# Kernel tuning notes

Hardware: AMD Instinct MI355X
Metric: run time of the kernel (lower is better)

The kernel has to match this reference:

```python
import jax, jax.numpy as jnp
import numpy as np


def setup_inputs() -> dict:
    key = jax.random.key(0)
    ks = jax.random.split(key, 8)
    B, N, A, H = 2, 2048, 256, 8
    KD = A // H  # key_dim per head = 32
    VD = A // H  # value_dim per head = 32
    return {
        "q_data": jax.random.normal(ks[0], (B, N, A), dtype=jnp.float32),
        "bias": jax.random.normal(ks[1], (B, N), dtype=jnp.float32),
        "nonbatched_bias": jax.random.normal(ks[2], (H, N, N), dtype=jnp.float32),
        "query_w": jax.random.normal(ks[3], (A, H, KD), dtype=jnp.float32) * 0.05,
        "query_b": jax.random.normal(ks[4], (1, H, KD), dtype=jnp.float32) * 0.05,
        "key_w": jax.random.normal(ks[5], (A, H, KD), dtype=jnp.float32) * 0.05,
        "value_w": jax.random.normal(ks[6], (A, H, VD), dtype=jnp.float32) * 0.05,
        "gating_w": jax.random.normal(ks[7], (A, H, VD), dtype=jnp.float32) * 0.05,
    }


def reference(q_data, bias, nonbatched_bias, query_w, query_b, key_w, value_w, gating_w):
    # q_data: [b, n, a]; bias: [b, n_k]; nonbatched_bias: [h, n_q, n_k]
    key_dim = query_w.shape[-1]
    scale = key_dim ** (-0.5)
    # projections (fused QKV in the original kernel)
    q = (jnp.einsum("bqa,ahc->bqhc", q_data, query_w) + query_b) * scale  # [b,q,h,c]
    k = jnp.einsum("bka,ahc->bkhc", q_data, key_w)                        # [b,k,h,c]
    v = jnp.einsum("bka,ahv->bkhv", q_data, value_w)                      # [b,k,h,v]
    # attention logits + batched bias (over keys) + shared nonbatched bias
    logits = jnp.einsum("bqhc,bkhc->bhqk", q, k)
    logits = logits + bias[:, None, None, :] + nonbatched_bias[None]
    weights = jax.nn.softmax(logits, axis=-1)                             # [b,h,q,k]
    weighted = jnp.einsum("bhqk,bkhv->bqhv", weights, v)                  # [b,q,h,v]
    # sigmoid gating branch fused after value projection
    gate = jax.nn.sigmoid(jnp.einsum("bqa,ahv->bqhv", q_data, gating_w))
    return weighted * gate                                                # [b,q,h,v]
```

## Files before the change

### kernel.cpp

```cpp
#include <hip/hip_runtime.h>
#include <stdint.h>

#define NTOK 2048
#define SCALE 0.17677669529663687f

typedef short s16x8 __attribute__((ext_vector_type(8)));
typedef unsigned short u16x8 __attribute__((ext_vector_type(8)));
typedef float f32x4 __attribute__((ext_vector_type(4)));

__device__ __forceinline__ unsigned short f2bf(float f) {
  unsigned int u = __builtin_bit_cast(unsigned int, f);
  u += 0x7fffu + ((u >> 16) & 1u);
  return (unsigned short)(u >> 16);
}

__global__ __launch_bounds__(256) void prep_weights_k(
    const float* __restrict__ qw, const float* __restrict__ kw,
    const float* __restrict__ vw, const float* __restrict__ gw,
    unsigned short* __restrict__ Wt) {
  __shared__ float tile[64][68];
  const int p = blockIdx.z;
  const int a0 = blockIdx.x * 64;
  const int n0 = blockIdx.y * 64;
  const float* src = (p == 0) ? qw : (p == 1) ? kw : (p == 2) ? vw : gw;
  const int tx = threadIdx.x & 15;
  const int ty = threadIdx.x >> 4;
#pragma unroll
  for (int kk = 0; kk < 4; kk++) {
    int ar = ty + kk * 16;
    float4 v = *reinterpret_cast<const float4*>(src + (a0 + ar) * 256 + n0 + tx * 4);
    tile[ar][tx * 4 + 0] = v.x; tile[ar][tx * 4 + 1] = v.y;
    tile[ar][tx * 4 + 2] = v.z; tile[ar][tx * 4 + 3] = v.w;
  }
  __syncthreads();
  unsigned short* dst = Wt + p * 65536;
#pragma unroll
  for (int kk = 0; kk < 4; kk++) {
    int nr = ty + kk * 16;
    ushort4 o;
    o.x = f2bf(tile[tx * 4 + 0][nr]);
    o.y = f2bf(tile[tx * 4 + 1][nr]);
    o.z = f2bf(tile[tx * 4 + 2][nr]);
    o.w = f2bf(tile[tx * 4 + 3][nr]);
    *reinterpret_cast<ushort4*>(dst + (n0 + nr) * 256 + a0 + tx * 4) = o;
  }
}

__global__ __launch_bounds__(256) void proj_k(
    const float* __restrict__ x, const unsigned short* __restrict__ Wt,
    const float* __restrict__ query_b,
    unsigned short* __restrict__ Qg, unsigned short* __restrict__ Kg,
    unsigned short* __restrict__ Vt, float* __restrict__ gate) {
  const int w = threadIdx.x >> 6;
  const int lane = threadIdx.x & 63;
  const int l15 = lane & 15;
  const int quad = lane >> 4;
  const int p = blockIdx.y >> 1;
  const int half = blockIdx.y & 1;
  const int rbase = blockIdx.x * 128 + w * 32;
  const unsigned short* wp = Wt + p * 65536;

  f32x4 acc[2][8];
#pragma unroll
  for (int rt = 0; rt < 2; rt++)
#pragma unroll
    for (int ct = 0; ct < 8; ct++) acc[rt][ct] = (f32x4){0.f, 0.f, 0.f, 0.f};

  for (int ks = 0; ks < 8; ks++) {
    const int kb = ks * 32;
    s16x8 af[2];
#pragma unroll
    for (int rt = 0; rt < 2; rt++) {
      const float* xr = x + (rbase + rt * 16 + l15) * 256 + kb + quad * 8;
      float4 f0 = *reinterpret_cast<const float4*>(xr);
      float4 f1 = *reinterpret_cast<const float4*>(xr + 4);
      u16x8 t;
      t[0] = f2bf(f0.x); t[1] = f2bf(f0.y); t[2] = f2bf(f0.z); t[3] = f2bf(f0.w);
      t[4] = f2bf(f1.x); t[5] = f2bf(f1.y); t[6] = f2bf(f1.z); t[7] = f2bf(f1.w);
      af[rt] = __builtin_bit_cast(s16x8, t);
    }
#pragma unroll
    for (int ct = 0; ct < 8; ct++) {
      uint4 bv = *reinterpret_cast<const uint4*>(
          wp + (half * 128 + ct * 16 + l15) * 256 + kb + quad * 8);
      s16x8 bfr = __builtin_bit_cast(s16x8, bv);
#pragma unroll
      for (int rt = 0; rt < 2; rt++)
        acc[rt][ct] = __builtin_amdgcn_mfma_f32_16x16x32_bf16(af[rt], bfr, acc[rt][ct], 0, 0, 0);
    }
  }

#pragma unroll
  for (int ct = 0; ct < 8; ct++) {
    const int cgl = half * 128 + ct * 16 + l15;
    const int h = cgl >> 5, c = cgl & 31;
#pragma unroll
    for (int rt = 0; rt < 2; rt++) {
      const int n0r = rbase + rt * 16 + quad * 4;
      const int bidx = n0r >> 11;
      const int nl0 = n0r & 2047;
      if (p == 0) {
        const float qb = query_b[cgl];
#pragma unroll
        for (int i = 0; i < 4; i++) {
          float v = (acc[rt][ct][i] + qb) * SCALE;
          Qg[(size_t)((bidx * 8 + h) * 2048 + nl0 + i) * 32 + c] = f2bf(v);
        }
      } else if (p == 1) {
#pragma unroll
        for (int i = 0; i < 4; i++)
          Kg[(size_t)((bidx * 8 + h) * 2048 + nl0 + i) * 32 + c] = f2bf(acc[rt][ct][i]);
      } else if (p == 2) {
        ushort4 o;
        o.x = f2bf(acc[rt][ct][0]); o.y = f2bf(acc[rt][ct][1]);
        o.z = f2bf(acc[rt][ct][2]); o.w = f2bf(acc[rt][ct][3]);
        *reinterpret_cast<ushort4*>(Vt + (size_t)((bidx * 8 + h) * 32 + c) * 2048 + nl0) = o;
      } else {
#pragma unroll
        for (int i = 0; i < 4; i++) {
          float s = 1.f / (1.f + __expf(-acc[rt][ct][i]));
          gate[(size_t)(bidx * 2048 + nl0 + i) * 256 + cgl] = s;
        }
      }
    }
  }
}

#define PST 136
__global__ __launch_bounds__(128) void attn_k(
    const unsigned short* __restrict__ Qg, const unsigned short* __restrict__ Kg,
    const unsigned short* __restrict__ Vt, const float* __restrict__ bias,
    const float* __restrict__ nb, const float* __restrict__ gate,
    float* __restrict__ out) {
  __shared__ unsigned short Ps[2 * 32 * PST];
  const int w = threadIdx.x >> 6;
  const int lane = threadIdx.x & 63;
  const int l15 = lane & 15;
  const int quad = lane >> 4;
  const int h = blockIdx.y, b = blockIdx.z;
  const int bh = b * 8 + h;
  const int qbase = blockIdx.x * 64 + w * 32;
  const unsigned short* Qp = Qg + (size_t)bh * 2048 * 32;
  const unsigned short* Kp = Kg + (size_t)bh * 2048 * 32;
  const unsigned short* Vp = Vt + (size_t)bh * 32 * 2048;
  const float* nbp = nb + (size_t)h * 2048 * 2048;
  const float* biasp = bias + b * 2048;
  unsigned short* Pw = Ps + w * 32 * PST;

  s16x8 aq[2];
#pragma unroll
  for (int rt = 0; rt < 2; rt++)
    aq[rt] = __builtin_bit_cast(s16x8, *reinterpret_cast<const uint4*>(
        Qp + (size_t)(qbase + rt * 16 + l15) * 32 + quad * 8));

  float mst[2][4], lst[2][4];
  f32x4 o[2][2];
#pragma unroll
  for (int rt = 0; rt < 2; rt++)
#pragma unroll
    for (int i = 0; i < 4; i++) { mst[rt][i] = -INFINITY; lst[rt][i] = 0.f; }
#pragma unroll
  for (int rt = 0; rt < 2; rt++)
#pragma unroll
    for (int vt = 0; vt < 2; vt++) o[rt][vt] = (f32x4){0.f, 0.f, 0.f, 0.f};

  for (int kt = 0; kt < 16; kt++) {
    const int kb = kt * 128;
    s16x8 bk[8];
#pragma unroll
    for (int ct = 0; ct < 8; ct++)
      bk[ct] = __builtin_bit_cast(s16x8, *reinterpret_cast<const uint4*>(
          Kp + (size_t)(kb + ct * 16 + l15) * 32 + quad * 8));
    f32x4 s[2][8];
#pragma unroll
    for (int rt = 0; rt < 2; rt++)
#pragma unroll
      for (int ct = 0; ct < 8; ct++)
        s[rt][ct] = __builtin_amdgcn_mfma_f32_16x16x32_bf16(
            aq[rt], bk[ct], (f32x4){0.f, 0.f, 0.f, 0.f}, 0, 0, 0);

    float bcol[8];
#pragma unroll
    for (int ct = 0; ct < 8; ct++) bcol[ct] = biasp[kb + ct * 16 + l15];

#pragma unroll
    for (int rt = 0; rt < 2; rt++) {
      const int qr0 = qbase + rt * 16 + quad * 4;
      float nbv[8][4];
#pragma unroll
      for (int ct = 0; ct < 8; ct++)
#pragma unroll
        for (int i = 0; i < 4; i++)
          nbv[ct][i] = nbp[(size_t)(qr0 + i) * 2048 + kb + ct * 16 + l15];
#pragma unroll
      for (int ct = 0; ct < 8; ct++)
#pragma unroll
        for (int i = 0; i < 4; i++) s[rt][ct][i] += bcol[ct] + nbv[ct][i];

      float alpha[4];
#pragma unroll
      for (int i = 0; i < 4; i++) {
        float mx = s[rt][0][i];
#pragma unroll
        for (int ct = 1; ct < 8; ct++) mx = fmaxf(mx, s[rt][ct][i]);
        mx = fmaxf(mx, __shfl_xor(mx, 1));
        mx = fmaxf(mx, __shfl_xor(mx, 2));
        mx = fmaxf(mx, __shfl_xor(mx, 4));
        mx = fmaxf(mx, __shfl_xor(mx, 8));
        float mn = fmaxf(mst[rt][i], mx);
        alpha[i] = __expf(mst[rt][i] - mn);
        mst[rt][i] = mn;
        float sum = 0.f;
#pragma unroll
        for (int ct = 0; ct < 8; ct++) {
          float pv = __expf(s[rt][ct][i] - mn);
          Pw[(rt * 16 + quad * 4 + i) * PST + ct * 16 + l15] = f2bf(pv);
          sum += pv;
        }
        sum += __shfl_xor(sum, 1);
        sum += __shfl_xor(sum, 2);
        sum += __shfl_xor(sum, 4);
        sum += __shfl_xor(sum, 8);
        lst[rt][i] = lst[rt][i] * alpha[i] + sum;
      }
#pragma unroll
      for (int vt = 0; vt < 2; vt++)
#pragma unroll
        for (int i = 0; i < 4; i++) o[rt][vt][i] *= alpha[i];
    }

    s16x8 vbf[4][2];
#pragma unroll
    for (int kc = 0; kc < 4; kc++)
#pragma unroll
      for (int vt = 0; vt < 2; vt++)
        vbf[kc][vt] = __builtin_bit_cast(s16x8, *reinterpret_cast<const uint4*>(
            Vp + (size_t)(vt * 16 + l15) * 2048 + kb + kc * 32 + quad * 8));
#pragma unroll
    for (int rt = 0; rt < 2; rt++)
#pragma unroll
      for (int kc = 0; kc < 4; kc++) {
        s16x8 ap = __builtin_bit_cast(s16x8, *reinterpret_cast<const uint4*>(
            &Pw[(rt * 16 + l15) * PST + kc * 32 + quad * 8]));
#pragma unroll
        for (int vt = 0; vt < 2; vt++)
          o[rt][vt] = __builtin_amdgcn_mfma_f32_16x16x32_bf16(ap, vbf[kc][vt], o[rt][vt], 0, 0, 0);
      }
  }

#pragma unroll
  for (int rt = 0; rt < 2; rt++) {
    const int qr0 = qbase + rt * 16 + quad * 4;
#pragma unroll
    for (int vt = 0; vt < 2; vt++)
#pragma unroll
      for (int i = 0; i < 4; i++) {
        const int q = qr0 + i;
        const int v = vt * 16 + l15;
        const size_t oidx = (size_t)(b * 2048 + q) * 256 + h * 32 + v;
        out[oidx] = (o[rt][vt][i] / lst[rt][i]) * gate[oidx];
      }
  }
}

extern "C" void kernel_launch(void* const* d_in, const int* in_sizes, int n_in,
                              void* d_out, int out_size, void* d_ws, size_t ws_size,
                              hipStream_t stream) {
  const float* q_data = (const float*)d_in[0];
  const float* bias = (const float*)d_in[1];
  const float* nbb = (const float*)d_in[2];
  const float* qw = (const float*)d_in[3];
  const float* qb = (const float*)d_in[4];
  const float* kw = (const float*)d_in[5];
  const float* vw = (const float*)d_in[6];
  const float* gw = (const float*)d_in[7];
  float* out = (float*)d_out;

  char* ws = (char*)d_ws;
  unsigned short* Wt = (unsigned short*)(ws + 0);
  unsigned short* Qg = (unsigned short*)(ws + 524288);
  unsigned short* Kg = (unsigned short*)(ws + 2621440);
  unsigned short* Vt = (unsigned short*)(ws + 4718592);
  float* gate = (float*)(ws + 6815744);

  prep_weights_k<<<dim3(4, 4, 4), 256, 0, stream>>>(qw, kw, vw, gw, Wt);
  proj_k<<<dim3(32, 8), 256, 0, stream>>>(q_data, Wt, qb, Qg, Kg, Vt, gate);
  attn_k<<<dim3(32, 8, 2), 128, 0, stream>>>(Qg, Kg, Vt, bias, nbb, gate, out);
}
```

Baseline: 282.5 us.

## Halve rows per wave and prefetch bias tiles in attention kernel

Each wave now processes 16 query rows instead of 32 and the grid doubles, raising the number of resident waves. The bias and nonbatched-bias values for the next key tile are loaded into a register double-buffer while the current tile is computed, hiding global load latency on the dominant nb stream. The cost is doubled K/V reloads per query row and more registers for the prefetch buffers.

```diff
diff --git a/kernel.cpp b/kernel.cpp
--- a/kernel.cpp
+++ b/kernel.cpp
@@ -127,107 +127,74 @@
 }
 
 #define PST 136
-__global__ __launch_bounds__(128) void attn_k(
+__global__ __launch_bounds__(128, 2) void attn_k(
     const unsigned short* __restrict__ Qg, const unsigned short* __restrict__ Kg,
     const unsigned short* __restrict__ Vt, const float* __restrict__ bias,
     const float* __restrict__ nb, const float* __restrict__ gate,
     float* __restrict__ out) {
-  __shared__ unsigned short Ps[2 * 32 * PST];
+  __shared__ unsigned short Ps[2 * 16 * PST];
   const int w = threadIdx.x >> 6;
   const int lane = threadIdx.x & 63;
   const int l15 = lane & 15;
   const int quad = lane >> 4;
   const int h = blockIdx.y, b = blockIdx.z;
   const int bh = b * 8 + h;
-  const int qbase = blockIdx.x * 64 + w * 32;
+  const int qbase = blockIdx.x * 32 + w * 16;
   const unsigned short* Qp = Qg + (size_t)bh * 2048 * 32;
   const unsigned short* Kp = Kg + (size_t)bh * 2048 * 32;
   const unsigned short* Vp = Vt + (size_t)bh * 32 * 2048;
   const float* nbp = nb + (size_t)h * 2048 * 2048;
   const float* biasp = bias + b * 2048;
-  unsigned short* Pw = Ps + w * 32 * PST;
-
-  s16x8 aq[2];
-#pragma unroll
-  for (int rt = 0; rt < 2; rt++)
-    aq[rt] = __builtin_bit_cast(s16x8, *reinterpret_cast<const uint4*>(
-        Qp + (size_t)(qbase + rt * 16 + l15) * 32 + quad * 8));
-
-  float mst[2][4], lst[2][4];
-  f32x4 o[2][2];
-#pragma unroll
-  for (int rt = 0; rt < 2; rt++)
-#pragma unroll
-    for (int i = 0; i < 4; i++) { mst[rt][i] = -INFINITY; lst[rt][i] = 0.f; }
-#pragma unroll
-  for (int rt = 0; rt < 2; rt++)
-#pragma unroll
-    for (int vt = 0; vt < 2; vt++) o[rt][vt] = (f32x4){0.f, 0.f, 0.f, 0.f};
-
+  unsigned short* Pw = Ps + w * 16 * PST;
+
+  s16x8 aq = __builtin_bit_cast(s16x8, *reinterpret_cast<const uint4*>(
+      Qp + (size_t)(qbase + l15) * 32 + quad * 8));
+  const int qr0 = qbase + quad * 4;
+
+  float mst[4], lst[4];
+  f32x4 o[2];
+#pragma unroll
+  for (int i = 0; i < 4; i++) { mst[i] = -INFINITY; lst[i] = 0.f; }
+#pragma unroll
+  for (int vt = 0; vt < 2; vt++) o[vt] = (f32x4){0.f, 0.f, 0.f, 0.f};
+
+  float nbuf[2][32];
+  float bb[2][8];
+#pragma unroll
+  for (int ct = 0; ct < 8; ct++) {
+    bb[0][ct] = biasp[ct * 16 + l15];
+#pragma unroll
+    for (int i = 0; i < 4; i++)
+      nbuf[0][ct * 4 + i] = nbp[(size_t)(qr0 + i) * 2048 + ct * 16 + l15];
+  }
+
+#pragma unroll 2
   for (int kt = 0; kt < 16; kt++) {
     const int kb = kt * 128;
+    const int cur = kt & 1, nxt = cur ^ 1;
+
     s16x8 bk[8];
 #pragma unroll
     for (int ct = 0; ct < 8; ct++)
       bk[ct] = __builtin_bit_cast(s16x8, *reinterpret_cast<const uint4*>(
           Kp + (size_t)(kb + ct * 16 + l15) * 32 + quad * 8));
-    f32x4 s[2][8];
-#pragma unroll
-    for (int rt = 0; rt < 2; rt++)
-#pragma unroll
-      for (int ct = 0; ct < 8; ct++)
-        s[rt][ct] = __builtin_amdgcn_mfma_f32_16x16x32_bf16(
-            aq[rt], bk[ct], (f32x4){0.f, 0.f, 0.f, 0.f}, 0, 0, 0);
-
-    float bcol[8];
-#pragma unroll
-    for (int ct = 0; ct < 8; ct++) bcol[ct] = biasp[kb + ct * 16 + l15];
-
-#pragma unroll
-    for (int rt = 0; rt < 2; rt++) {
-      const int qr0 = qbase + rt * 16 + quad * 4;
-      float nbv[8][4];
-#pragma unroll
-      for (int ct = 0; ct < 8; ct++)
+
+    if (kt < 15) {
+      const int kb2 = kb + 128;
+#pragma unroll
+      for (int ct = 0; ct < 8; ct++) {
+        bb[nxt][ct] = biasp[kb2 + ct * 16 + l15];
 #pragma unroll
         for (int i = 0; i < 4; i++)
-          nbv[ct][i] = nbp[(size_t)(qr0 + i) * 2048 + kb + ct * 16 + l15];
-#pragma unroll
-      for (int ct = 0; ct < 8; ct++)
-#pragma unroll
-        for (int i = 0; i < 4; i++) s[rt][ct][i] += bcol[ct] + nbv[ct][i];
-
-      float alpha[4];
-#pragma unroll
-      for (int i = 0; i < 4; i++) {
-        float mx = s[rt][0][i];
-#pragma unroll
-        for (int ct = 1; ct < 8; ct++) mx = fmaxf(mx, s[rt][ct][i]);
-        mx = fmaxf(mx, __shfl_xor(mx, 1));
-        mx = fmaxf(mx, __shfl_xor(mx, 2));
-        mx = fmaxf(mx, __shfl_xor(mx, 4));
-        mx = fmaxf(mx, __shfl_xor(mx, 8));
-        float mn = fmaxf(mst[rt][i], mx);
-        alpha[i] = __expf(mst[rt][i] - mn);
-        mst[rt][i] = mn;
-        float sum = 0.f;
-#pragma unroll
-        for (int ct = 0; ct < 8; ct++) {
-          float pv = __expf(s[rt][ct][i] - mn);
-          Pw[(rt * 16 + quad * 4 + i) * PST + ct * 16 + l15] = f2bf(pv);
-          sum += pv;
-        }
-        sum += __shfl_xor(sum, 1);
-        sum += __shfl_xor(sum, 2);
-        sum += __shfl_xor(sum, 4);
-        sum += __shfl_xor(sum, 8);
-        lst[rt][i] = lst[rt][i] * alpha[i] + sum;
+          nbuf[nxt][ct * 4 + i] = nbp[(size_t)(qr0 + i) * 2048 + kb2 + ct * 16 + l15];
       }
-#pragma unroll
-      for (int vt = 0; vt < 2; vt++)
-#pragma unroll
-        for (int i = 0; i < 4; i++) o[rt][vt][i] *= alpha[i];
-    }
+    }
+
+    f32x4 s[8];
+#pragma unroll
+    for (int ct = 0; ct < 8; ct++)
+      s[ct] = __builtin_amdgcn_mfma_f32_16x16x32_bf16(
+          aq, bk[ct], (f32x4){0.f, 0.f, 0.f, 0.f}, 0, 0, 0);
 
     s16x8 vbf[4][2];
 #pragma unroll
@@ -236,31 +203,62 @@
       for (int vt = 0; vt < 2; vt++)
         vbf[kc][vt] = __builtin_bit_cast(s16x8, *reinterpret_cast<const uint4*>(
             Vp + (size_t)(vt * 16 + l15) * 2048 + kb + kc * 32 + quad * 8));
-#pragma unroll
-    for (int rt = 0; rt < 2; rt++)
-#pragma unroll
-      for (int kc = 0; kc < 4; kc++) {
-        s16x8 ap = __builtin_bit_cast(s16x8, *reinterpret_cast<const uint4*>(
-            &Pw[(rt * 16 + l15) * PST + kc * 32 + quad * 8]));
-#pragma unroll
-        for (int vt = 0; vt < 2; vt++)
-          o[rt][vt] = __builtin_amdgcn_mfma_f32_16x16x32_bf16(ap, vbf[kc][vt], o[rt][vt], 0, 0, 0);
+
+#pragma unroll
+    for (int ct = 0; ct < 8; ct++)
+#pragma unroll
+      for (int i = 0; i < 4; i++) s[ct][i] += bb[cur][ct] + nbuf[cur][ct * 4 + i];
+
+    float alpha[4];
+#pragma unroll
+    for (int i = 0; i < 4; i++) {
+      float mx = s[0][i];
+#pragma unroll
+      for (int ct = 1; ct < 8; ct++) mx = fmaxf(mx, s[ct][i]);
+      mx = fmaxf(mx, __shfl_xor(mx, 1));
+      mx = fmaxf(mx, __shfl_xor(mx, 2));
+      mx = fmaxf(mx, __shfl_xor(mx, 4));
+      mx = fmaxf(mx, __shfl_xor(mx, 8));
+      float mn = fmaxf(mst[i], mx);
+      alpha[i] = __expf(mst[i] - mn);
+      mst[i] = mn;
+      float sum = 0.f;
+#pragma unroll
+      for (int ct = 0; ct < 8; ct++) {
+        float pv = __expf(s[ct][i] - mn);
+        Pw[(quad * 4 + i) * PST + ct * 16 + l15] = f2bf(pv);
+        sum += pv;
       }
-  }
-
-#pragma unroll
-  for (int rt = 0; rt < 2; rt++) {
-    const int qr0 = qbase + rt * 16 + quad * 4;
+      sum += __shfl_xor(sum, 1);
+      sum += __shfl_xor(sum, 2);
+      sum += __shfl_xor(sum, 4);
+      sum += __shfl_xor(sum, 8);
+      lst[i] = lst[i] * alpha[i] + sum;
+    }
 #pragma unroll
     for (int vt = 0; vt < 2; vt++)
 #pragma unroll
-      for (int i = 0; i < 4; i++) {
-        const int q = qr0 + i;
-        const int v = vt * 16 + l15;
-        const size_t oidx = (size_t)(b * 2048 + q) * 256 + h * 32 + v;
-        out[oidx] = (o[rt][vt][i] / lst[rt][i]) * gate[oidx];
-      }
-  }
+      for (int i = 0; i < 4; i++) o[vt][i] *= alpha[i];
+
+#pragma unroll
+    for (int kc = 0; kc < 4; kc++) {
+      s16x8 ap = __builtin_bit_cast(s16x8, *reinterpret_cast<const uint4*>(
+          &Pw[l15 * PST + kc * 32 + quad * 8]));
+#pragma unroll
+      for (int vt = 0; vt < 2; vt++)
+        o[vt] = __builtin_amdgcn_mfma_f32_16x16x32_bf16(ap, vbf[kc][vt], o[vt], 0, 0, 0);
+    }
+  }
+
+#pragma unroll
+  for (int vt = 0; vt < 2; vt++)
+#pragma unroll
+    for (int i = 0; i < 4; i++) {
+      const int q = qr0 + i;
+      const int v = vt * 16 + l15;
+      const size_t oidx = (size_t)(b * 2048 + q) * 256 + h * 32 + v;
+      out[oidx] = (o[vt][i] / lst[i]) * gate[oidx];
+    }
 }
 
 extern "C" void kernel_launch(void* const* d_in, const int* in_sizes, int n_in,
@@ -285,5 +283,5 @@
 
   prep_weights_k<<<dim3(4, 4, 4), 256, 0, stream>>>(qw, kw, vw, gw, Wt);
   proj_k<<<dim3(32, 8), 256, 0, stream>>>(q_data, Wt, qb, Qg, Kg, Vt, gate);
-  attn_k<<<dim3(32, 8, 2), 128, 0, stream>>>(Qg, Kg, Vt, bias, nbb, gate, out);
-}
+  attn_k<<<dim3(64, 8, 2), 128, 0, stream>>>(Qg, Kg, Vt, bias, nbb, gate, out);
+}
```

New measurement: 261.0 us. 7.6% less time.
